# Kernel optimization log

Measured on AMD Instinct MI355X. Metric: run time of the kernel, lower is better.

The kernel has to match this reference:

```python
import jax, jax.numpy as jnp
import numpy as np

V, E, C = 50000, 5000, 16
TAU = 0.5
EPS = 1e-08
SPARSITY = 0.02  # fraction of (v,e) incidences


def setup_inputs() -> dict:
    key = jax.random.key(0)
    k1, k2, k3, k4 = jax.random.split(key, 4)
    pred_s = jax.random.normal(k1, (V, C), dtype=jnp.float32)
    pred_t = jax.random.normal(k2, (V, C), dtype=jnp.float32)
    # binary incidence matrix; pin vertex 0 into every edge so deg_e > 0
    H = (jax.random.uniform(k3, (V, E)) < SPARSITY).astype(jnp.float32)
    H = H.at[0, :].set(1.0)
    e_mask = jax.random.randint(k4, (E,), 0, 2).astype(jnp.bool_)
    return {"pred_s": pred_s, "pred_t": pred_t, "H": H, "e_mask": e_mask}


def _v2e_mean(p, H, deg_e):
    # == einsum('vc,ve->ec', p, H @ diag(1/deg_e)) : column-normalized scatter-mean
    return jnp.einsum('ve,vc->ec', H, p) / deg_e[:, None]


def reference(pred_s, pred_t, H, e_mask):
    ps = jax.nn.softmax(pred_s, axis=1)   # [V, C]
    pt = jax.nn.softmax(pred_t, axis=1)   # [V, C]
    deg_e = H.sum(axis=0)                 # [E]
    log_s = jnp.log(_v2e_mean(ps, H, deg_e) / TAU + EPS)  # [E, C]
    log_t = jnp.log(_v2e_mean(pt, H, deg_e) / TAU + EPS)  # [E, C]
    # F.kl_div(input=log_s, target=log_t, log_target=True, reduction='batchmean')
    # restricted to masked edges; mask via weights to keep shapes static.
    kl = jnp.exp(log_t) * (log_t - log_s)                  # [E, C]
    m = e_mask.astype(kl.dtype)                            # [E]
    n_sel = jnp.maximum(m.sum(), 1.0)
    return (kl * m[:, None]).sum() / n_sel
```

## Files before the change

### kernel.cpp

```cpp
#include <hip/hip_runtime.h>

#define NV 50000
#define NE 5000
#define NC 16
#define TAU_INV 2.0f
#define EPS 1e-8f

#define NCH 100
#define VCH 500
#define GRP 4
#define NXB 5
#define NBLK (NXB * NCH)
#define NLANE 5120

typedef float vf4 __attribute__((ext_vector_type(4)));

__global__ __launch_bounds__(256) void softmax_kernel(
    const float* __restrict__ pred_s, const float* __restrict__ pred_t,
    float* __restrict__ p) {
  int i = blockIdx.x * 256 + threadIdx.x;
  if (i >= 2 * NV) return;
  const float* src;
  float* dst;
  if (i < NV) { src = pred_s + (size_t)i * NC; dst = p + (size_t)i * 32; }
  else        { int j = i - NV; src = pred_t + (size_t)j * NC; dst = p + (size_t)j * 32 + 16; }
  float4 a = ((const float4*)src)[0];
  float4 b = ((const float4*)src)[1];
  float4 c = ((const float4*)src)[2];
  float4 d = ((const float4*)src)[3];
  float x[16] = {a.x,a.y,a.z,a.w, b.x,b.y,b.z,b.w, c.x,c.y,c.z,c.w, d.x,d.y,d.z,d.w};
  float mx = x[0];
#pragma unroll
  for (int k = 1; k < 16; ++k) mx = fmaxf(mx, x[k]);
  float sum = 0.f;
#pragma unroll
  for (int k = 0; k < 16; ++k) { x[k] = expf(x[k] - mx); sum += x[k]; }
  float inv = 1.f / sum;
#pragma unroll
  for (int k = 0; k < 16; ++k) x[k] *= inv;
  float4 o0 = {x[0], x[1], x[2], x[3]};
  float4 o1 = {x[4], x[5], x[6], x[7]};
  float4 o2 = {x[8], x[9], x[10], x[11]};
  float4 o3 = {x[12], x[13], x[14], x[15]};
  ((float4*)dst)[0] = o0;
  ((float4*)dst)[1] = o1;
  ((float4*)dst)[2] = o2;
  ((float4*)dst)[3] = o3;
}

__global__ __launch_bounds__(256) void accum_kernel(
    const float* __restrict__ H, const float* __restrict__ p,
    float* __restrict__ part) {
  __shared__ float lp[VCH * 32];
  int b = blockIdx.x;
  int item;
  if (b < 496) item = (b & 7) * 62 + (b >> 3);
  else         item = b;
  int xb = item % NXB;
  int y  = item / NXB;
  int e0 = 4 * (xb * 256 + (int)threadIdx.x);
  if (e0 > NE - 4) e0 = NE - 4;
  int v0 = y * VCH;

  {
    const float4* __restrict__ src = (const float4*)(p + (size_t)v0 * 32);
    float4* dst = (float4*)lp;
    for (int i = threadIdx.x; i < VCH * 8; i += 256) dst[i] = src[i];
  }
  __syncthreads();

  float4 aS[16], aT[16], dg;
#pragma unroll
  for (int k = 0; k < 16; ++k) {
    aS[k] = make_float4(0.f, 0.f, 0.f, 0.f);
    aT[k] = make_float4(0.f, 0.f, 0.f, 0.f);
  }
  dg = make_float4(0.f, 0.f, 0.f, 0.f);

  const float* __restrict__ hp = H + (size_t)v0 * NE + e0;

  vf4 hc[GRP];
#pragma unroll
  for (int u = 0; u < GRP; ++u)
    hc[u] = *(const vf4*)(hp + (size_t)u * NE);

  for (int vb = 0; vb < VCH; vb += GRP) {
    int nb = (vb + GRP < VCH) ? vb + GRP : vb;
    vf4 hn[GRP];
#pragma unroll
    for (int u = 0; u < GRP; ++u)
      hn[u] = *(const vf4*)(hp + (size_t)(nb + u) * NE);

#pragma unroll
    for (int u = 0; u < GRP; ++u) {
      const float4* __restrict__ r = (const float4*)(lp + (size_t)(vb + u) * 32);
      vf4 h = hc[u];
      dg.x += h.x; dg.y += h.y; dg.z += h.z; dg.w += h.w;
      {
        float4 s0 = r[0], s1 = r[1], s2 = r[2], s3 = r[3];
        float sv[16] = {s0.x,s0.y,s0.z,s0.w, s1.x,s1.y,s1.z,s1.w,
                        s2.x,s2.y,s2.z,s2.w, s3.x,s3.y,s3.z,s3.w};
#pragma unroll
        for (int k = 0; k < 16; ++k) {
          aS[k].x = fmaf(h.x, sv[k], aS[k].x);
          aS[k].y = fmaf(h.y, sv[k], aS[k].y);
          aS[k].z = fmaf(h.z, sv[k], aS[k].z);
          aS[k].w = fmaf(h.w, sv[k], aS[k].w);
        }
      }
      {
        float4 t0 = r[4], t1 = r[5], t2 = r[6], t3 = r[7];
        float tv[16] = {t0.x,t0.y,t0.z,t0.w, t1.x,t1.y,t1.z,t1.w,
                        t2.x,t2.y,t2.z,t2.w, t3.x,t3.y,t3.z,t3.w};
#pragma unroll
        for (int k = 0; k < 16; ++k) {
          aT[k].x = fmaf(h.x, tv[k], aT[k].x);
          aT[k].y = fmaf(h.y, tv[k], aT[k].y);
          aT[k].z = fmaf(h.z, tv[k], aT[k].z);
          aT[k].w = fmaf(h.w, tv[k], aT[k].w);
        }
      }
    }
#pragma unroll
    for (int u = 0; u < GRP; ++u) hc[u] = hn[u];
  }

  float* op = part + (size_t)y * 33 * NLANE + e0;
#pragma unroll
  for (int k = 0; k < 16; ++k) {
    vf4 w = {aS[k].x, aS[k].y, aS[k].z, aS[k].w};
    *(vf4*)(op + (size_t)k * NLANE) = w;
  }
#pragma unroll
  for (int k = 0; k < 16; ++k) {
    vf4 w = {aT[k].x, aT[k].y, aT[k].z, aT[k].w};
    *(vf4*)(op + (size_t)(16 + k) * NLANE) = w;
  }
  {
    vf4 w = {dg.x, dg.y, dg.z, dg.w};
    *(vf4*)(op + (size_t)32 * NLANE) = w;
  }
}

__global__ __launch_bounds__(256) void reduce_kernel(
    const float* __restrict__ part, float* __restrict__ acc) {
  int i = blockIdx.x * 256 + threadIdx.x;
  if (i >= 33 * NLANE) return;
  float s = 0.f;
#pragma unroll 4
  for (int y = 0; y < NCH; ++y)
    s += part[(size_t)y * 33 * NLANE + i];
  acc[i] = s;
}

__global__ __launch_bounds__(256) void kl_kernel(
    const float* __restrict__ acc, const unsigned char* __restrict__ e_mask,
    float* __restrict__ out) {
  __shared__ float snum[4];
  __shared__ float scnt[4];
  int t = threadIdx.x;
  float num = 0.f, cnt = 0.f;
  for (int e = t; e < NE; e += 256) {
    if (e_mask[e]) {
      float deg = acc[(size_t)32 * NLANE + e];
      float invd = 1.f / deg;
      float kl = 0.f;
#pragma unroll
      for (int k = 0; k < 16; ++k) {
        float ms = acc[(size_t)k * NLANE + e] * invd;
        float mt = acc[(size_t)(16 + k) * NLANE + e] * invd;
        float xs = ms * TAU_INV + EPS;
        float xt = mt * TAU_INV + EPS;
        kl += xt * (logf(xt) - logf(xs));
      }
      num += kl;
      cnt += 1.f;
    }
  }
#pragma unroll
  for (int off = 32; off > 0; off >>= 1) {
    num += __shfl_down(num, off, 64);
    cnt += __shfl_down(cnt, off, 64);
  }
  if ((t & 63) == 0) { snum[t >> 6] = num; scnt[t >> 6] = cnt; }
  __syncthreads();
  if (t == 0) {
    float n = snum[0] + snum[1] + snum[2] + snum[3];
    float c2 = scnt[0] + scnt[1] + scnt[2] + scnt[3];
    out[0] = n / fmaxf(c2, 1.f);
  }
}

extern "C" void kernel_launch(void* const* d_in, const int* in_sizes, int n_in,
                              void* d_out, int out_size, void* d_ws, size_t ws_size,
                              hipStream_t stream) {
  const float* pred_s = (const float*)d_in[0];
  const float* pred_t = (const float*)d_in[1];
  const float* H      = (const float*)d_in[2];
  const unsigned char* e_mask = (const unsigned char*)d_in[3];

  float* ws   = (float*)d_ws;
  float* p    = ws;
  float* acc  = ws + (size_t)NV * 32;
  float* part = acc + (size_t)33 * NLANE;

  softmax_kernel<<<dim3((2 * NV + 255) / 256), 256, 0, stream>>>(pred_s, pred_t, p);
  accum_kernel<<<dim3(NBLK), 256, 0, stream>>>(H, p, part);
  reduce_kernel<<<dim3((33 * NLANE + 255) / 256), 256, 0, stream>>>(part, acc);
  kl_kernel<<<1, 256, 0, stream>>>(acc, e_mask, (float*)d_out);
}
```

Baseline: 1.354 ms.

## Compress incidence matrix to uint8 before accumulation and double-buffer row loads

```diff
diff --git a/kernel.cpp b/kernel.cpp
--- a/kernel.cpp
+++ b/kernel.cpp
@@ -2,13 +2,14 @@
 
 #define NV 50000
 #define NE 5000
+#define NE8 5120
 #define NC 16
 #define TAU_INV 2.0f
 #define EPS 1e-8f
 
 #define NCH 100
 #define VCH 500
-#define GRP 4
+#define GRP 5
 #define NXB 5
 #define NBLK (NXB * NCH)
 #define NLANE 5120
@@ -48,8 +49,59 @@
   ((float4*)dst)[3] = o3;
 }
 
+__global__ __launch_bounds__(256) void compress_kernel(
+    const float* __restrict__ H, unsigned char* __restrict__ H8) {
+  for (int row = blockIdx.x; row < NV; row += gridDim.x) {
+    const float* src = H + (size_t)row * NE;
+    unsigned char* dst = H8 + (size_t)row * NE8;
+    for (int u = threadIdx.x; u < 625; u += 256) {
+      vf4 a = __builtin_nontemporal_load((const vf4*)(src + (size_t)u * 8));
+      vf4 b = __builtin_nontemporal_load((const vf4*)(src + (size_t)u * 8 + 4));
+      uint x0 = (uint)(a.x != 0.f) | ((uint)(a.y != 0.f) << 8) |
+                ((uint)(a.z != 0.f) << 16) | ((uint)(a.w != 0.f) << 24);
+      uint x1 = (uint)(b.x != 0.f) | ((uint)(b.y != 0.f) << 8) |
+                ((uint)(b.z != 0.f) << 16) | ((uint)(b.w != 0.f) << 24);
+      uint2 w; w.x = x0; w.y = x1;
+      *(uint2*)(dst + (size_t)u * 8) = w;
+    }
+  }
+}
+
+#define ROW_BODY(ROW, HW) {                                                  \
+    const float4* __restrict__ r = (const float4*)(lp + (size_t)(ROW) * 32); \
+    float hx = (float)((HW) & 255u);                                         \
+    float hy = (float)(((HW) >> 8) & 255u);                                  \
+    float hz = (float)(((HW) >> 16) & 255u);                                 \
+    float hw_ = (float)((HW) >> 24);                                         \
+    dg.x += hx; dg.y += hy; dg.z += hz; dg.w += hw_;                         \
+    {                                                                        \
+      float4 s0 = r[0], s1 = r[1], s2 = r[2], s3 = r[3];                     \
+      float sv[16] = {s0.x,s0.y,s0.z,s0.w, s1.x,s1.y,s1.z,s1.w,              \
+                      s2.x,s2.y,s2.z,s2.w, s3.x,s3.y,s3.z,s3.w};             \
+      _Pragma("unroll")                                                      \
+      for (int k = 0; k < 16; ++k) {                                         \
+        aS[k].x = fmaf(hx, sv[k], aS[k].x);                                  \
+        aS[k].y = fmaf(hy, sv[k], aS[k].y);                                  \
+        aS[k].z = fmaf(hz, sv[k], aS[k].z);                                  \
+        aS[k].w = fmaf(hw_, sv[k], aS[k].w);                                 \
+      }                                                                      \
+    }                                                                        \
+    {                                                                        \
+      float4 t0 = r[4], t1 = r[5], t2 = r[6], t3 = r[7];                     \
+      float tv[16] = {t0.x,t0.y,t0.z,t0.w, t1.x,t1.y,t1.z,t1.w,              \
+                      t2.x,t2.y,t2.z,t2.w, t3.x,t3.y,t3.z,t3.w};             \
+      _Pragma("unroll")                                                      \
+      for (int k = 0; k < 16; ++k) {                                         \
+        aT[k].x = fmaf(hx, tv[k], aT[k].x);                                  \
+        aT[k].y = fmaf(hy, tv[k], aT[k].y);                                  \
+        aT[k].z = fmaf(hz, tv[k], aT[k].z);                                  \
+        aT[k].w = fmaf(hw_, tv[k], aT[k].w);                                 \
+      }                                                                      \
+    }                                                                        \
+  }
+
 __global__ __launch_bounds__(256) void accum_kernel(
-    const float* __restrict__ H, const float* __restrict__ p,
+    const unsigned char* __restrict__ H8, const float* __restrict__ p,
     float* __restrict__ part) {
   __shared__ float lp[VCH * 32];
   int b = blockIdx.x;
@@ -77,52 +129,33 @@
   }
   dg = make_float4(0.f, 0.f, 0.f, 0.f);
 
-  const float* __restrict__ hp = H + (size_t)v0 * NE + e0;
-
-  vf4 hc[GRP];
+  const unsigned char* __restrict__ hp = H8 + (size_t)v0 * NE8 + e0;
+
+  uint hA[GRP], hB[GRP];
 #pragma unroll
   for (int u = 0; u < GRP; ++u)
-    hc[u] = *(const vf4*)(hp + (size_t)u * NE);
-
-  for (int vb = 0; vb < VCH; vb += GRP) {
-    int nb = (vb + GRP < VCH) ? vb + GRP : vb;
-    vf4 hn[GRP];
-#pragma unroll
-    for (int u = 0; u < GRP; ++u)
-      hn[u] = *(const vf4*)(hp + (size_t)(nb + u) * NE);
-
-#pragma unroll
-    for (int u = 0; u < GRP; ++u) {
-      const float4* __restrict__ r = (const float4*)(lp + (size_t)(vb + u) * 32);
-      vf4 h = hc[u];
-      dg.x += h.x; dg.y += h.y; dg.z += h.z; dg.w += h.w;
-      {
-        float4 s0 = r[0], s1 = r[1], s2 = r[2], s3 = r[3];
-        float sv[16] = {s0.x,s0.y,s0.z,s0.w, s1.x,s1.y,s1.z,s1.w,
-                        s2.x,s2.y,s2.z,s2.w, s3.x,s3.y,s3.z,s3.w};
-#pragma unroll
-        for (int k = 0; k < 16; ++k) {
-          aS[k].x = fmaf(h.x, sv[k], aS[k].x);
-          aS[k].y = fmaf(h.y, sv[k], aS[k].y);
-          aS[k].z = fmaf(h.z, sv[k], aS[k].z);
-          aS[k].w = fmaf(h.w, sv[k], aS[k].w);
-        }
-      }
-      {
-        float4 t0 = r[4], t1 = r[5], t2 = r[6], t3 = r[7];
-        float tv[16] = {t0.x,t0.y,t0.z,t0.w, t1.x,t1.y,t1.z,t1.w,
-                        t2.x,t2.y,t2.z,t2.w, t3.x,t3.y,t3.z,t3.w};
-#pragma unroll
-        for (int k = 0; k < 16; ++k) {
-          aT[k].x = fmaf(h.x, tv[k], aT[k].x);
-          aT[k].y = fmaf(h.y, tv[k], aT[k].y);
-          aT[k].z = fmaf(h.z, tv[k], aT[k].z);
-          aT[k].w = fmaf(h.w, tv[k], aT[k].w);
-        }
-      }
-    }
-#pragma unroll
-    for (int u = 0; u < GRP; ++u) hc[u] = hn[u];
+    hA[u] = *(const uint*)(hp + (size_t)u * NE8);
+#pragma unroll
+  for (int u = 0; u < GRP; ++u)
+    hB[u] = *(const uint*)(hp + (size_t)(GRP + u) * NE8);
+
+  for (int vb = 0; vb < VCH; vb += 2 * GRP) {
+#pragma unroll
+    for (int u = 0; u < GRP; ++u) ROW_BODY(vb + u, hA[u])
+    {
+      int nb = vb + 2 * GRP; if (nb > VCH - GRP) nb = VCH - GRP;
+#pragma unroll
+      for (int u = 0; u < GRP; ++u)
+        hA[u] = *(const uint*)(hp + (size_t)(nb + u) * NE8);
+    }
+#pragma unroll
+    for (int u = 0; u < GRP; ++u) ROW_BODY(vb + GRP + u, hB[u])
+    {
+      int nb = vb + 3 * GRP; if (nb > VCH - GRP) nb = VCH - GRP;
+#pragma unroll
+      for (int u = 0; u < GRP; ++u)
+        hB[u] = *(const uint*)(hp + (size_t)(nb + u) * NE8);
+    }
   }
 
   float* op = part + (size_t)y * 33 * NLANE + e0;
@@ -203,9 +236,11 @@
   float* p    = ws;
   float* acc  = ws + (size_t)NV * 32;
   float* part = acc + (size_t)33 * NLANE;
+  unsigned char* H8 = (unsigned char*)(part + (size_t)NCH * 33 * NLANE);
 
   softmax_kernel<<<dim3((2 * NV + 255) / 256), 256, 0, stream>>>(pred_s, pred_t, p);
-  accum_kernel<<<dim3(NBLK), 256, 0, stream>>>(H, p, part);
+  compress_kernel<<<dim3(2048), 256, 0, stream>>>(H, H8);
+  accum_kernel<<<dim3(NBLK), 256, 0, stream>>>(H8, p, part);
   reduce_kernel<<<dim3((33 * NLANE + 255) / 256), 256, 0, stream>>>(part, acc);
   kl_kernel<<<1, 256, 0, stream>>>(acc, e_mask, (float*)d_out);
 }
```

New measurement: 1.721 ms. 1.27x slower.

## Fuse partial reduction and KL into one kernel, use nontemporal H loads

Applied to the files above, without the earlier changes.

```diff
diff --git a/kernel.cpp b/kernel.cpp
--- a/kernel.cpp
+++ b/kernel.cpp
@@ -8,17 +8,19 @@
 
 #define NCH 100
 #define VCH 500
-#define GRP 4
+#define GRP 2
 #define NXB 5
 #define NBLK (NXB * NCH)
 #define NLANE 5120
+#define FB 80
 
 typedef float vf4 __attribute__((ext_vector_type(4)));
 
 __global__ __launch_bounds__(256) void softmax_kernel(
     const float* __restrict__ pred_s, const float* __restrict__ pred_t,
-    float* __restrict__ p) {
+    float* __restrict__ p, float* __restrict__ scal) {
   int i = blockIdx.x * 256 + threadIdx.x;
+  if (i == 0) { scal[0] = 0.f; scal[1] = 0.f; scal[2] = 0.f; }
   if (i >= 2 * NV) return;
   const float* src;
   float* dst;
@@ -82,14 +84,14 @@
   vf4 hc[GRP];
 #pragma unroll
   for (int u = 0; u < GRP; ++u)
-    hc[u] = *(const vf4*)(hp + (size_t)u * NE);
+    hc[u] = __builtin_nontemporal_load((const vf4*)(hp + (size_t)u * NE));
 
   for (int vb = 0; vb < VCH; vb += GRP) {
     int nb = (vb + GRP < VCH) ? vb + GRP : vb;
     vf4 hn[GRP];
 #pragma unroll
     for (int u = 0; u < GRP; ++u)
-      hn[u] = *(const vf4*)(hp + (size_t)(nb + u) * NE);
+      hn[u] = __builtin_nontemporal_load((const vf4*)(hp + (size_t)(nb + u) * NE));
 
 #pragma unroll
     for (int u = 0; u < GRP; ++u) {
@@ -142,52 +144,61 @@
   }
 }
 
-__global__ __launch_bounds__(256) void reduce_kernel(
-    const float* __restrict__ part, float* __restrict__ acc) {
-  int i = blockIdx.x * 256 + threadIdx.x;
-  if (i >= 33 * NLANE) return;
-  float s = 0.f;
-#pragma unroll 4
-  for (int y = 0; y < NCH; ++y)
-    s += part[(size_t)y * 33 * NLANE + i];
-  acc[i] = s;
-}
-
-__global__ __launch_bounds__(256) void kl_kernel(
-    const float* __restrict__ acc, const unsigned char* __restrict__ e_mask,
-    float* __restrict__ out) {
-  __shared__ float snum[4];
-  __shared__ float scnt[4];
+__global__ __launch_bounds__(1024) void finale_kernel(
+    const float* __restrict__ part, const unsigned char* __restrict__ e_mask,
+    float* __restrict__ scal, float* __restrict__ out) {
+  __shared__ float sl[33 * 64];
   int t = threadIdx.x;
-  float num = 0.f, cnt = 0.f;
-  for (int e = t; e < NE; e += 256) {
-    if (e_mask[e]) {
-      float deg = acc[(size_t)32 * NLANE + e];
+  int el = t & 63, yq = t >> 6;
+  int e = blockIdx.x * 64 + el;
+
+  float a[33];
+#pragma unroll
+  for (int k = 0; k < 33; ++k) a[k] = 0.f;
+  for (int y = yq; y < NCH; y += 16) {
+    const float* __restrict__ bp = part + (size_t)y * 33 * NLANE + e;
+#pragma unroll
+    for (int k = 0; k < 33; ++k) a[k] += bp[(size_t)k * NLANE];
+  }
+
+  for (int i = t; i < 33 * 64; i += 1024) sl[i] = 0.f;
+  __syncthreads();
+#pragma unroll
+  for (int k = 0; k < 33; ++k) atomicAdd(&sl[k * 64 + el], a[k]);
+  __syncthreads();
+
+  if (t < 64) {
+    float num = 0.f, cntv = 0.f;
+    if (e < NE && e_mask[e]) {
+      float deg = sl[32 * 64 + el];
       float invd = 1.f / deg;
       float kl = 0.f;
 #pragma unroll
       for (int k = 0; k < 16; ++k) {
-        float ms = acc[(size_t)k * NLANE + e] * invd;
-        float mt = acc[(size_t)(16 + k) * NLANE + e] * invd;
+        float ms = sl[k * 64 + el] * invd;
+        float mt = sl[(16 + k) * 64 + el] * invd;
         float xs = ms * TAU_INV + EPS;
         float xt = mt * TAU_INV + EPS;
         kl += xt * (logf(xt) - logf(xs));
       }
-      num += kl;
-      cnt += 1.f;
-    }
-  }
-#pragma unroll
-  for (int off = 32; off > 0; off >>= 1) {
-    num += __shfl_down(num, off, 64);
-    cnt += __shfl_down(cnt, off, 64);
-  }
-  if ((t & 63) == 0) { snum[t >> 6] = num; scnt[t >> 6] = cnt; }
-  __syncthreads();
-  if (t == 0) {
-    float n = snum[0] + snum[1] + snum[2] + snum[3];
-    float c2 = scnt[0] + scnt[1] + scnt[2] + scnt[3];
-    out[0] = n / fmaxf(c2, 1.f);
+      num = kl; cntv = 1.f;
+    }
+#pragma unroll
+    for (int off = 32; off > 0; off >>= 1) {
+      num += __shfl_down(num, off, 64);
+      cntv += __shfl_down(cntv, off, 64);
+    }
+    if (t == 0) {
+      atomicAdd(&scal[0], num);
+      atomicAdd(&scal[1], cntv);
+      __threadfence();
+      unsigned int tk = atomicAdd((unsigned int*)&scal[2], 1u);
+      if (tk == FB - 1) {
+        float n = atomicAdd(&scal[0], 0.f);
+        float c = atomicAdd(&scal[1], 0.f);
+        out[0] = n / fmaxf(c, 1.f);
+      }
+    }
   }
 }
 
@@ -201,11 +212,10 @@
 
   float* ws   = (float*)d_ws;
   float* p    = ws;
-  float* acc  = ws + (size_t)NV * 32;
-  float* part = acc + (size_t)33 * NLANE;
-
-  softmax_kernel<<<dim3((2 * NV + 255) / 256), 256, 0, stream>>>(pred_s, pred_t, p);
+  float* part = p + (size_t)NV * 32;
+  float* scal = part + (size_t)NCH * 33 * NLANE;
+
+  softmax_kernel<<<dim3((2 * NV + 255) / 256), 256, 0, stream>>>(pred_s, pred_t, p, scal);
   accum_kernel<<<dim3(NBLK), 256, 0, stream>>>(H, p, part);
-  reduce_kernel<<<dim3((33 * NLANE + 255) / 256), 256, 0, stream>>>(part, acc);
-  kl_kernel<<<1, 256, 0, stream>>>(acc, e_mask, (float*)d_out);
-}
+  finale_kernel<<<dim3(FB), 1024, 0, stream>>>(part, e_mask, scal, (float*)d_out);
+}
```

New measurement: 1.346 ms, median of 2. No clear change (-0.5%).
